# Performance work log

Hardware: AMD Instinct MI355X
Metric: run time of the kernel (lower is better)

## Reference

```python
import jax, jax.numpy as jnp
import numpy as np

N = 50000
E = 600000
D_IN = 128
D_OUT = 128
LN_EPS = 1e-5


def setup_inputs() -> dict:
    key = jax.random.key(0)
    k_h, k_src, k_dst, k_w, k_b, k_g, k_bt = jax.random.split(key, 7)
    h = jax.random.normal(k_h, (N, D_IN), dtype=jnp.float32)
    src = jax.random.randint(k_src, (E,), 0, N, dtype=jnp.int64)
    dst = jax.random.randint(k_dst, (E,), 0, N, dtype=jnp.int64)
    edge_index = jnp.stack([src, dst], axis=0)
    # nn.Linear default init: U(-1/sqrt(in), 1/sqrt(in))
    bound = 1.0 / np.sqrt(D_IN)
    W = jax.random.uniform(k_w, (D_OUT, D_IN), jnp.float32, -bound, bound)
    b = jax.random.uniform(k_b, (D_OUT,), jnp.float32, -bound, bound)
    gamma = jnp.ones((D_OUT,), dtype=jnp.float32)
    beta = jnp.zeros((D_OUT,), dtype=jnp.float32)
    return {"h": h, "edge_index": edge_index, "W": W, "b": b,
            "gamma": gamma, "beta": beta}


def reference(h, edge_index, W, b, gamma, beta):
    src, dst = edge_index[0], edge_index[1]
    # scatter_add of gathered neighbor features: agg[dst] += h[src]
    agg = jax.ops.segment_sum(h[src], dst, num_segments=N)  # [N, D_IN]
    x = agg + h
    # Linear
    y = x @ W.T + b  # [N, D_OUT]
    # LayerNorm over last dim
    mu = jnp.mean(y, axis=-1, keepdims=True)
    var = jnp.mean(jnp.square(y - mu), axis=-1, keepdims=True)
    y = (y - mu) / jnp.sqrt(var + LN_EPS) * gamma + beta
    # ReLU; Dropout is identity in eval mode
    return jax.nn.relu(y)
```

## Files before the change

kernel.cpp:

```cpp
#include <hip/hip_runtime.h>
#include <hip/hip_bf16.h>

#define D 128
#define LN_EPS 1e-5f
#define MAXSLOT 64

typedef __attribute__((ext_vector_type(8))) short bf16x8s;
typedef __attribute__((ext_vector_type(4))) float f32x4;

__device__ inline unsigned pack2_bf16(float x, float y) {
    __hip_bfloat16 b0 = __float2bfloat16(x);
    __hip_bfloat16 b1 = __float2bfloat16(y);
    unsigned short u0, u1;
    __builtin_memcpy(&u0, &b0, 2);
    __builtin_memcpy(&u1, &b1, 2);
    return (unsigned)u0 | ((unsigned)u1 << 16);
}
__device__ inline float bf16lo(unsigned u) { return __uint_as_float(u << 16); }
__device__ inline float bf16hi(unsigned u) { return __uint_as_float(u & 0xffff0000u); }

__global__ __launch_bounds__(256) void prep_kernel(
    const float* __restrict__ W, const float* __restrict__ h,
    unsigned short* __restrict__ w_bf, unsigned* __restrict__ h_bf,
    int* __restrict__ cnt, int N)
{
    const int tid    = blockIdx.x * blockDim.x + threadIdx.x;
    const int stride = gridDim.x * blockDim.x;
    for (int i = tid; i < D * D; i += stride) {
        __hip_bfloat16 v = __float2bfloat16(W[i]);
        unsigned short u; __builtin_memcpy(&u, &v, 2);
        w_bf[i] = u;
    }
    const float2* h2 = (const float2*)h;
    const int nh = N * (D / 2);
    for (int i = tid; i < nh; i += stride) {
        float2 v = h2[i];
        h_bf[i] = pack2_bf16(v.x, v.y);
    }
    for (int i = tid; i < D / 2; i += stride)
        h_bf[(N << 6) + i] = 0u;
    for (int i = tid; i < N; i += stride) cnt[i] = 0;
}

__global__ __launch_bounds__(256) void fill_kernel(
    const int* __restrict__ src, const int* __restrict__ dst,
    int* __restrict__ cnt, int* __restrict__ slots, int E)
{
    int e = blockIdx.x * blockDim.x + threadIdx.x;
    if (e < E) {
        int d   = dst[e];
        int pos = atomicAdd(&cnt[d], 1);
        if (pos < MAXSLOT) slots[(d << 6) + pos] = src[e];
    }
}

__global__ __launch_bounds__(256) void gather_kernel(
    const uint2* __restrict__ h2,
    const int*   __restrict__ cnt,
    const int*   __restrict__ slots,
    uint2*       __restrict__ x2,
    int N)
{
    const int lane = threadIdx.x & 63;
    const int half = lane >> 5;
    const int col  = lane & 31;
    const int wid  = blockIdx.x * (blockDim.x >> 6) + (threadIdx.x >> 6);
    const int nw   = gridDim.x * (blockDim.x >> 6);

    for (int n = wid; n < N; n += nw) {
        int deg = cnt[n];
        if (deg > MAXSLOT) deg = MAXSLOT;
        int idx = (lane < deg) ? slots[(n << 6) + lane] : N;
        uint2 self = h2[((size_t)n << 5) + col];

        float f0 = 0.f, f1 = 0.f, f2 = 0.f, f3 = 0.f;
        const int pairs = (deg + 1) >> 1;
        int q = 0;
        for (; q + 3 < pairs; q += 4) {
            uint2 u[4];
            #pragma unroll
            for (int t = 0; t < 4; ++t) {
                int r = __shfl(idx, ((q + t) << 1) | half, 64);
                u[t] = h2[((size_t)r << 5) + col];
            }
            #pragma unroll
            for (int t = 0; t < 4; ++t) {
                f0 += bf16lo(u[t].x); f1 += bf16hi(u[t].x);
                f2 += bf16lo(u[t].y); f3 += bf16hi(u[t].y);
            }
        }
        for (; q < pairs; ++q) {
            int r = __shfl(idx, (q << 1) | half, 64);
            uint2 u0 = h2[((size_t)r << 5) + col];
            f0 += bf16lo(u0.x); f1 += bf16hi(u0.x);
            f2 += bf16lo(u0.y); f3 += bf16hi(u0.y);
        }

        f0 += __shfl_xor(f0, 32, 64);
        f1 += __shfl_xor(f1, 32, 64);
        f2 += __shfl_xor(f2, 32, 64);
        f3 += __shfl_xor(f3, 32, 64);
        if (half == 0) {
            f0 += bf16lo(self.x); f1 += bf16hi(self.x);
            f2 += bf16lo(self.y); f3 += bf16hi(self.y);
            uint2 o;
            o.x = pack2_bf16(f0, f1);
            o.y = pack2_bf16(f2, f3);
            x2[((size_t)n << 5) + col] = o;
        }
    }
}

__global__ __launch_bounds__(256) void gemm_ln_kernel(
    const unsigned short* __restrict__ x_bf,
    const unsigned short* __restrict__ w_bf,
    const float* __restrict__ bias,
    const float* __restrict__ gamma,
    const float* __restrict__ beta,
    float*       __restrict__ out,
    int N)
{
    const int lane   = threadIdx.x & 63;
    const int row16  = lane & 15;
    const int kgrp   = lane >> 4;
    const int base_n = ((blockIdx.x << 2) | (threadIdx.x >> 6)) << 5;
    if (base_n >= N) return;

    float bj[8], gj[8], bej[8];
    #pragma unroll
    for (int jt = 0; jt < 8; ++jt) {
        int j = (jt << 4) + row16;
        bj[jt]  = bias[j];
        gj[jt]  = gamma[j];
        bej[jt] = beta[j];
    }

    bf16x8s a[2][4];
    #pragma unroll
    for (int sub = 0; sub < 2; ++sub) {
        int r = base_n + (sub << 4) + row16;
        if (r >= N) r = N - 1;
        const bf16x8s* xp = (const bf16x8s*)(x_bf + ((size_t)r << 7));
        #pragma unroll
        for (int kt = 0; kt < 4; ++kt)
            a[sub][kt] = xp[(kt << 2) + kgrp];
    }

    f32x4 acc[2][8] = {};
    #pragma unroll
    for (int kt = 0; kt < 4; ++kt) {
        #pragma unroll
        for (int jt = 0; jt < 8; ++jt) {
            const bf16x8s* wp = (const bf16x8s*)(w_bf + (((jt << 4) + row16) << 7));
            bf16x8s bfrag = wp[(kt << 2) + kgrp];
            acc[0][jt] = __builtin_amdgcn_mfma_f32_16x16x32_bf16(
                a[0][kt], bfrag, acc[0][jt], 0, 0, 0);
            acc[1][jt] = __builtin_amdgcn_mfma_f32_16x16x32_bf16(
                a[1][kt], bfrag, acc[1][jt], 0, 0, 0);
        }
    }

    #pragma unroll
    for (int sub = 0; sub < 2; ++sub) {
        #pragma unroll
        for (int jt = 0; jt < 8; ++jt)
            #pragma unroll
            for (int r = 0; r < 4; ++r)
                acc[sub][jt][r] += bj[jt];

        float s[4], s2[4];
        #pragma unroll
        for (int r = 0; r < 4; ++r) {
            float ls = 0.f, ls2 = 0.f;
            #pragma unroll
            for (int jt = 0; jt < 8; ++jt) {
                float v = acc[sub][jt][r];
                ls  += v;
                ls2 += v * v;
            }
            #pragma unroll
            for (int m = 1; m < 16; m <<= 1) {
                ls  += __shfl_xor(ls,  m, 64);
                ls2 += __shfl_xor(ls2, m, 64);
            }
            s[r] = ls; s2[r] = ls2;
        }

        #pragma unroll
        for (int r = 0; r < 4; ++r) {
            int n = base_n + (sub << 4) + (kgrp << 2) + r;
            if (n >= N) continue;
            float mu   = s[r]  * (1.0f / D);
            float var  = s2[r] * (1.0f / D) - mu * mu;
            float rstd = rsqrtf(var + LN_EPS);
            float* op  = out + ((size_t)n << 7);
            #pragma unroll
            for (int jt = 0; jt < 8; ++jt) {
                float o = (acc[sub][jt][r] - mu) * rstd * gj[jt] + bej[jt];
                op[(jt << 4) + row16] = fmaxf(o, 0.0f);
            }
        }
    }
}

extern "C" void kernel_launch(void* const* d_in, const int* in_sizes, int n_in,
                              void* d_out, int out_size, void* d_ws, size_t ws_size,
                              hipStream_t stream) {
    const float* h     = (const float*)d_in[0];
    const int*   eidx  = (const int*)  d_in[1];
    const float* W     = (const float*)d_in[2];
    const float* b     = (const float*)d_in[3];
    const float* gamma = (const float*)d_in[4];
    const float* beta  = (const float*)d_in[5];
    float*       out   = (float*)d_out;

    const int N = in_sizes[0] / D;
    const int E = in_sizes[1] / 2;
    const int* src = eidx;
    const int* dst = eidx + E;

    char* ws = (char*)d_ws;
    int* cnt   = (int*)ws;                               ws += (size_t)N * 4;
    ws = (char*)(((size_t)ws + 255) & ~(size_t)255);
    int* slots = (int*)ws;                               ws += (size_t)N * MAXSLOT * 4;
    ws = (char*)(((size_t)ws + 255) & ~(size_t)255);
    unsigned short* w_bf = (unsigned short*)ws;          ws += (size_t)D * D * 2;
    ws = (char*)(((size_t)ws + 255) & ~(size_t)255);
    unsigned* h_bf = (unsigned*)ws;                      ws += ((size_t)N + 1) * D * 2;
    ws = (char*)(((size_t)ws + 255) & ~(size_t)255);
    unsigned* x_bf = (unsigned*)ws;

    prep_kernel<<<1024, 256, 0, stream>>>(W, h, w_bf, h_bf, cnt, N);
    fill_kernel<<<(E + 255) / 256, 256, 0, stream>>>(src, dst, cnt, slots, E);
    gather_kernel<<<2048, 256, 0, stream>>>(
        (const uint2*)h_bf, cnt, slots, (uint2*)x_bf, N);
    gemm_ln_kernel<<<(N + 127) / 128, 256, 0, stream>>>(
        (const unsigned short*)x_bf, w_bf, b, gamma, beta, out, N);
}
```

Measured before the change: 157.6 us.

## Fuse gather into GEMM+LayerNorm via LDS and merge prep with edge fill

The neighbor gather now writes each wave's 32 aggregated rows into a swizzled shared-memory tile, which the MFMA GEMM + LayerNorm then reads directly, removing the global write and re-read of the intermediate x buffer. The edge bucketing is folded into the prep kernel and count zeroing moves to a memset, cutting two launches. In exchange the fused kernel runs only about 400 blocks, each wave gathering 32 rows serially, so there is less parallelism to hide gather latency. The merged prep kernel also runs the atomic fill and the bf16 conversion in the same blocks.

```diff
diff --git a/kernel.cpp b/kernel.cpp
--- a/kernel.cpp
+++ b/kernel.cpp
@@ -19,13 +19,21 @@
 __device__ inline float bf16lo(unsigned u) { return __uint_as_float(u << 16); }
 __device__ inline float bf16hi(unsigned u) { return __uint_as_float(u & 0xffff0000u); }
 
-__global__ __launch_bounds__(256) void prep_kernel(
+__global__ __launch_bounds__(256) void prep_fill_kernel(
     const float* __restrict__ W, const float* __restrict__ h,
+    const int* __restrict__ src, const int* __restrict__ dst,
     unsigned short* __restrict__ w_bf, unsigned* __restrict__ h_bf,
-    int* __restrict__ cnt, int N)
+    int* __restrict__ cnt, int* __restrict__ slots,
+    int N, int E)
 {
     const int tid    = blockIdx.x * blockDim.x + threadIdx.x;
     const int stride = gridDim.x * blockDim.x;
+
+    for (int e = tid; e < E; e += stride) {
+        int d   = dst[e];
+        int pos = atomicAdd(&cnt[d], 1);
+        if (pos < MAXSLOT) slots[(d << 6) + pos] = src[e];
+    }
     for (int i = tid; i < D * D; i += stride) {
         __hip_bfloat16 v = __float2bfloat16(W[i]);
         unsigned short u; __builtin_memcpy(&u, &v, 2);
@@ -39,35 +47,35 @@
     }
     for (int i = tid; i < D / 2; i += stride)
         h_bf[(N << 6) + i] = 0u;
-    for (int i = tid; i < N; i += stride) cnt[i] = 0;
-}
-
-__global__ __launch_bounds__(256) void fill_kernel(
-    const int* __restrict__ src, const int* __restrict__ dst,
-    int* __restrict__ cnt, int* __restrict__ slots, int E)
-{
-    int e = blockIdx.x * blockDim.x + threadIdx.x;
-    if (e < E) {
-        int d   = dst[e];
-        int pos = atomicAdd(&cnt[d], 1);
-        if (pos < MAXSLOT) slots[(d << 6) + pos] = src[e];
-    }
-}
-
-__global__ __launch_bounds__(256) void gather_kernel(
-    const uint2* __restrict__ h2,
-    const int*   __restrict__ cnt,
-    const int*   __restrict__ slots,
-    uint2*       __restrict__ x2,
+}
+
+__global__ __launch_bounds__(256) void gather_gemm_kernel(
+    const uint2*          __restrict__ h2,
+    const int*            __restrict__ cnt,
+    const int*            __restrict__ slots,
+    const unsigned short* __restrict__ w_bf,
+    const float* __restrict__ bias,
+    const float* __restrict__ gamma,
+    const float* __restrict__ beta,
+    float*       __restrict__ out,
     int N)
 {
-    const int lane = threadIdx.x & 63;
-    const int half = lane >> 5;
-    const int col  = lane & 31;
-    const int wid  = blockIdx.x * (blockDim.x >> 6) + (threadIdx.x >> 6);
-    const int nw   = gridDim.x * (blockDim.x >> 6);
-
-    for (int n = wid; n < N; n += nw) {
+    __shared__ uint2 xs[4][32][32];
+
+    const int wv     = threadIdx.x >> 6;
+    const int lane   = threadIdx.x & 63;
+    const int half   = lane >> 5;
+    const int col    = lane & 31;
+    const int base_n = ((blockIdx.x << 2) | wv) << 5;
+    if (base_n >= N) return;
+
+    for (int nn = 0; nn < 32; ++nn) {
+        const int n   = base_n + nn;
+        const int swc = col ^ ((nn & 7) << 1);
+        if (n >= N) {
+            if (half == 0) xs[wv][nn][swc] = make_uint2(0u, 0u);
+            continue;
+        }
         int deg = cnt[n];
         if (deg > MAXSLOT) deg = MAXSLOT;
         int idx = (lane < deg) ? slots[(n << 6) + lane] : N;
@@ -106,25 +114,12 @@
             uint2 o;
             o.x = pack2_bf16(f0, f1);
             o.y = pack2_bf16(f2, f3);
-            x2[((size_t)n << 5) + col] = o;
-        }
-    }
-}
-
-__global__ __launch_bounds__(256) void gemm_ln_kernel(
-    const unsigned short* __restrict__ x_bf,
-    const unsigned short* __restrict__ w_bf,
-    const float* __restrict__ bias,
-    const float* __restrict__ gamma,
-    const float* __restrict__ beta,
-    float*       __restrict__ out,
-    int N)
-{
-    const int lane   = threadIdx.x & 63;
-    const int row16  = lane & 15;
-    const int kgrp   = lane >> 4;
-    const int base_n = ((blockIdx.x << 2) | (threadIdx.x >> 6)) << 5;
-    if (base_n >= N) return;
+            xs[wv][nn][swc] = o;
+        }
+    }
+
+    const int row16 = lane & 15;
+    const int kgrp  = lane >> 4;
 
     float bj[8], gj[8], bej[8];
     #pragma unroll
@@ -138,12 +133,13 @@
     bf16x8s a[2][4];
     #pragma unroll
     for (int sub = 0; sub < 2; ++sub) {
-        int r = base_n + (sub << 4) + row16;
-        if (r >= N) r = N - 1;
-        const bf16x8s* xp = (const bf16x8s*)(x_bf + ((size_t)r << 7));
-        #pragma unroll
-        for (int kt = 0; kt < 4; ++kt)
-            a[sub][kt] = xp[(kt << 2) + kgrp];
+        const int rl = (sub << 4) + row16;
+        const int s  = (rl & 7) << 1;
+        #pragma unroll
+        for (int kt = 0; kt < 4; ++kt) {
+            const int c0 = (kt << 3) + (kgrp << 1);
+            a[sub][kt] = *(const bf16x8s*)&xs[wv][rl][c0 ^ s];
+        }
     }
 
     f32x4 acc[2][8] = {};
@@ -226,14 +222,11 @@
     ws = (char*)(((size_t)ws + 255) & ~(size_t)255);
     unsigned short* w_bf = (unsigned short*)ws;          ws += (size_t)D * D * 2;
     ws = (char*)(((size_t)ws + 255) & ~(size_t)255);
-    unsigned* h_bf = (unsigned*)ws;                      ws += ((size_t)N + 1) * D * 2;
-    ws = (char*)(((size_t)ws + 255) & ~(size_t)255);
-    unsigned* x_bf = (unsigned*)ws;
-
-    prep_kernel<<<1024, 256, 0, stream>>>(W, h, w_bf, h_bf, cnt, N);
-    fill_kernel<<<(E + 255) / 256, 256, 0, stream>>>(src, dst, cnt, slots, E);
-    gather_kernel<<<2048, 256, 0, stream>>>(
-        (const uint2*)h_bf, cnt, slots, (uint2*)x_bf, N);
-    gemm_ln_kernel<<<(N + 127) / 128, 256, 0, stream>>>(
-        (const unsigned short*)x_bf, w_bf, b, gamma, beta, out, N);
-}
+    unsigned* h_bf = (unsigned*)ws;
+
+    hipMemsetAsync(cnt, 0, (size_t)N * sizeof(int), stream);
+    prep_fill_kernel<<<2048, 256, 0, stream>>>(
+        W, h, src, dst, w_bf, h_bf, cnt, slots, N, E);
+    gather_gemm_kernel<<<(N + 127) / 128, 256, 0, stream>>>(
+        (const uint2*)h_bf, cnt, slots, w_bf, b, gamma, beta, out, N);
+}
```

New measurement: 190.3 us. 1.21x slower.
